# Kernel tuning notes

Hardware: AMD Instinct MI355X
Metric: run time of the kernel (lower is better)

The kernel has to match this reference:

```python
import jax, jax.numpy as jnp
import numpy as np

DN = ('NCHW', 'OIHW', 'NCHW')
COMMITMENT_COST = 0.25


def conv(x, w, b=None, stride=1, pad=0, groups=1):
    o = jax.lax.conv_general_dilated(x, w, (stride, stride), [(pad, pad), (pad, pad)],
                                     feature_group_count=groups, dimension_numbers=DN)
    return o if b is None else o + b[None, :, None, None]


def conv_t(x, w, b=None, stride=2, pad=1, groups=1):
    # w is in torch ConvTranspose2d layout: (in_ch, out_ch//groups, kH, kW)
    in_ch, outg, kh, kw = w.shape
    wf = jnp.flip(w, (-2, -1)).reshape(groups, in_ch // groups, outg, kh, kw)
    wf = wf.transpose(0, 2, 1, 3, 4).reshape(groups * outg, in_ch // groups, kh, kw)
    p = kh - 1 - pad
    o = jax.lax.conv_general_dilated(x, wf, (1, 1), [(p, p), (p, p)],
                                     lhs_dilation=(stride, stride),
                                     feature_group_count=groups, dimension_numbers=DN)
    return o if b is None else o + b[None, :, None, None]


def res_stack(x, w1, w2):
    # w1: (L, nrh, nh//2, 3, 3), w2: (L, nh, nrh//2, 1, 1); groups=2, no bias
    for i in range(w1.shape[0]):
        h = conv(jax.nn.relu(x), w1[i], pad=1, groups=2)
        h = conv(jax.nn.relu(h), w2[i], groups=2)
        x = x + h
    return jax.nn.relu(x)


def vq(z, emb, beta):
    # z: (B, C, H, W); emb: (K, C). EMA updates skipped (eval mode).
    zp = jnp.transpose(z, (0, 2, 3, 1))  # BHWC
    C = emb.shape[1]
    flat = zp.reshape(-1, C)
    d = (jnp.sum(flat ** 2, axis=1, keepdims=True)
         + jnp.sum(emb ** 2, axis=1) - 2.0 * flat @ emb.T)
    idx = jnp.argmin(d, axis=1)
    q = emb[idx].reshape(zp.shape)
    loss = beta * jnp.mean((jax.lax.stop_gradient(q) - zp) ** 2)
    q_st = zp + jax.lax.stop_gradient(q - zp)  # straight-through
    avg = jnp.mean(jax.nn.one_hot(idx, emb.shape[0], dtype=z.dtype), axis=0)
    perplexity = jnp.exp(-jnp.sum(avg * jnp.log(avg + 1e-10)))
    return loss, jnp.transpose(q_st, (0, 3, 1, 2)), perplexity


def _forward(x, eb_dw, eb_db, eb_rw, eb_rb, eb_c1w, eb_c1b, eb_c2w, eb_c2b, eb_c3w, eb_c3b,
             eb_rw1, eb_rw2, et_c1w, et_c1b, et_c2w, et_c2b, et_rw1, et_rw2,
             pvt_w, pvt_b, up_w, up_b, pvb_w, pvb_b, emb_t, emb_b,
             db_c1w, db_c1b, db_rw1, db_rw2, db_t1w, db_t1b, db_t2w, db_t2b,
             db_odw, db_odb, db_orw, db_orb):
    NH = eb_c3w.shape[0]
    ED = emb_t.shape[1]
    # --- EncoderBot ---
    xd = conv(x[:, :1], eb_dw, eb_db)      # depth 1x1 -> NH/4
    xr = conv(x[:, 1:], eb_rw, eb_rb)      # rgb 1x1 -> NH/4
    h = jax.nn.relu(jnp.concatenate([xd, xr], axis=1))
    h = jax.nn.relu(conv(h, eb_c1w, eb_c1b, stride=2, pad=1, groups=2))
    h = jax.nn.relu(conv(h, eb_c2w, eb_c2b, stride=2, pad=1, groups=2))
    h = conv(h, eb_c3w, eb_c3b, pad=1, groups=2)
    enc_b = res_stack(h, eb_rw1, eb_rw2)   # (B, NH, H/4, W/4)
    # --- EncoderTop ---
    t = jax.nn.relu(conv(enc_b, et_c1w, et_c1b, stride=2, pad=1, groups=2))
    t = jax.nn.relu(conv(t, et_c2w, et_c2b, pad=1, groups=2))
    enc_t = res_stack(t, et_rw1, et_rw2)   # (B, NH, H/8, W/8)
    # --- top VQ ---
    zt = conv(enc_t, pvt_w, pvt_b, groups=2)
    loss_t, q_t, perp_t = vq(zt, emb_t, COMMITMENT_COST)
    up_t = conv_t(q_t, up_w, up_b, stride=2, pad=1, groups=2)  # (B, ED, H/4, W/4)
    # --- PreVQBot: regroup channels as (enc_b_d, up_t_d, enc_b_rgb, up_t_rgb) ---
    joined = jnp.concatenate([enc_b[:, :NH // 2], up_t[:, :ED // 2],
                              enc_b[:, NH // 2:], up_t[:, ED // 2:]], axis=1)
    zb = conv(joined, pvb_w, pvb_b, groups=2)
    loss_b, q_b, perp_b = vq(zb, emb_b, COMMITMENT_COST)
    # --- DecoderBot: input cat(up_t, q_b), regrouped (t_d, b_d, t_rgb, b_rgb) ---
    dj = jnp.concatenate([up_t[:, :ED // 2], q_b[:, :ED // 2],
                          up_t[:, ED // 2:], q_b[:, ED // 2:]], axis=1)
    y = conv(dj, db_c1w, db_c1b, pad=1, groups=2)
    y = res_stack(y, db_rw1, db_rw2)
    y = jax.nn.relu(conv_t(y, db_t1w, db_t1b, stride=2, pad=1, groups=2))
    y = conv_t(y, db_t2w, db_t2b, stride=2, pad=1, groups=2)  # (B, NH/4, H, W), no relu
    c = y.shape[1]
    out_d = conv(y[:, :c // 2], db_odw, db_odb)
    out_rgb = conv(y[:, c // 2:], db_orw, db_orb)
    recon = jnp.concatenate([out_d, out_rgb], axis=1)  # (B, 4, H, W)
    return loss_b, loss_t, recon, q_t, q_b


def setup_inputs() -> dict:
    key = jax.random.key(0)
    NH, NRH, L, ED, K = 128, 64, 2, 128, 2048
    B, H, W = 8, 256, 256
    ks = iter(jax.random.split(key, 64))
    def w(*shape):
        return jax.random.normal(next(ks), shape, jnp.float32) * 0.05
    return dict(
        x=jax.random.normal(next(ks), (B, 4, H, W), jnp.float32),
        eb_dw=w(NH // 4, 1, 1, 1), eb_db=w(NH // 4),
        eb_rw=w(NH // 4, 3, 1, 1), eb_rb=w(NH // 4),
        eb_c1w=w(NH // 2, NH // 4, 4, 4), eb_c1b=w(NH // 2),
        eb_c2w=w(NH, NH // 4, 4, 4), eb_c2b=w(NH),
        eb_c3w=w(NH, NH // 2, 3, 3), eb_c3b=w(NH),
        eb_rw1=w(L, NRH, NH // 2, 3, 3), eb_rw2=w(L, NH, NRH // 2, 1, 1),
        et_c1w=w(NH, NH // 2, 4, 4), et_c1b=w(NH),
        et_c2w=w(NH, NH // 2, 3, 3), et_c2b=w(NH),
        et_rw1=w(L, NRH, NH // 2, 3, 3), et_rw2=w(L, NH, NRH // 2, 1, 1),
        pvt_w=w(ED, NH // 2, 1, 1), pvt_b=w(ED),
        up_w=w(ED, ED // 2, 4, 4), up_b=w(ED),
        pvb_w=w(ED, (NH + ED) // 2, 1, 1), pvb_b=w(ED),
        emb_t=jax.random.normal(next(ks), (K, ED), jnp.float32),
        emb_b=jax.random.normal(next(ks), (K, ED), jnp.float32),
        db_c1w=w(NH, ED, 3, 3), db_c1b=w(NH),
        db_rw1=w(L, NRH, NH // 2, 3, 3), db_rw2=w(L, NH, NRH // 2, 1, 1),
        db_t1w=w(NH, NH // 4, 4, 4), db_t1b=w(NH // 2),
        db_t2w=w(NH // 2, NH // 8, 4, 4), db_t2b=w(NH // 4),
        db_odw=w(1, NH // 8, 1, 1), db_odb=w(1),
        db_orw=w(3, NH // 8, 1, 1), db_orb=w(3),
    )


def reference(x, eb_dw, eb_db, eb_rw, eb_rb, eb_c1w, eb_c1b, eb_c2w, eb_c2b, eb_c3w, eb_c3b,
              eb_rw1, eb_rw2, et_c1w, et_c1b, et_c2w, et_c2b, et_rw1, et_rw2,
              pvt_w, pvt_b, up_w, up_b, pvb_w, pvb_b, emb_t, emb_b,
              db_c1w, db_c1b, db_rw1, db_rw2, db_t1w, db_t1b, db_t2w, db_t2b,
              db_odw, db_odb, db_orw, db_orb):
    return _forward(x, eb_dw, eb_db, eb_rw, eb_rb, eb_c1w, eb_c1b, eb_c2w, eb_c2b,
                    eb_c3w, eb_c3b, eb_rw1, eb_rw2, et_c1w, et_c1b, et_c2w, et_c2b,
                    et_rw1, et_rw2, pvt_w, pvt_b, up_w, up_b, pvb_w, pvb_b, emb_t, emb_b,
                    db_c1w, db_c1b, db_rw1, db_rw2, db_t1w, db_t1b, db_t2w, db_t2b,
                    db_odw, db_odb, db_orw, db_orb)
```

## Files before the change

### kernel.cpp

```cpp
#include <hip/hip_runtime.h>
#include <cstddef>

#define TPB 256

__device__ __forceinline__ float4 relu4(float4 v) {
    v.x = fmaxf(v.x, 0.0f); v.y = fmaxf(v.y, 0.0f);
    v.z = fmaxf(v.z, 0.0f); v.w = fmaxf(v.w, 0.0f);
    return v;
}

__device__ __forceinline__ const float* pick_src(const float* a, const float* b,
                                                 int n, int g, int l, int HW) {
    return (l < 64) ? a + ((size_t)n * 128 + g * 64 + l) * HW
                    : b + ((size_t)n * 128 + g * 64 + (l - 64)) * HW;
}

template<int W, int ROWS, int OCB, bool RELU_IN, bool SPLIT>
__global__ __launch_bounds__(256) void conv3_kernel(
    const float* __restrict__ in, const float* __restrict__ in2,
    const float* __restrict__ wgt, const float* __restrict__ bias,
    float* __restrict__ out, int Cin, int Cout, int relu_out)
{
    constexpr int J = ROWS * W / 64;
    constexpr int OCT = OCB * 4;
    constexpr int NW = OCB / 4;
    constexpr int ICB = 8;
    constexpr int IN_H = ROWS + 2, IN_W2 = W + 8;
    constexpr int W4 = W / 4;
    __shared__ float s_in[ICB][IN_H][IN_W2];
    __shared__ float s_w[ICB * 9 * OCT];

    const int tid = threadIdx.x;
    const int tx = tid & 63, ty = tid >> 6;
    const int n = blockIdx.z, oc0 = blockIdx.y * OCT, r0 = blockIdx.x * ROWS;
    const int icg = Cin >> 1, ocg = Cout >> 1;
    const int g = oc0 / ocg;

    float acc[OCB][J];
    #pragma unroll
    for (int o = 0; o < OCB; ++o) {
        const float b = bias ? bias[oc0 + ty * OCB + o] : 0.0f;
        #pragma unroll
        for (int j = 0; j < J; ++j) acc[o][j] = b;
    }

    const float* inb = SPLIT ? nullptr
                             : in + ((size_t)n * Cin + (size_t)g * icg) * (W * W);

    for (int ic0 = 0; ic0 < icg; ic0 += ICB) {
        __syncthreads();
        for (int i = tid; i < ICB * IN_H * W4; i += 256) {
            const int icl = i / (IN_H * W4);
            const int rem = i - icl * (IN_H * W4);
            const int rr = rem / W4, c4 = rem - rr * W4;
            const int y = r0 - 1 + rr;
            float4 v = make_float4(0.f, 0.f, 0.f, 0.f);
            if ((unsigned)y < (unsigned)W) {
                const float* src = SPLIT ? pick_src(in, in2, n, g, ic0 + icl, W * W)
                                         : inb + (size_t)(ic0 + icl) * (W * W);
                v = *(const float4*)(src + (size_t)y * W + 4 * c4);
            }
            if (RELU_IN) v = relu4(v);
            *(float4*)&s_in[icl][rr][4 + 4 * c4] = v;
        }
        for (int i = tid; i < ICB * IN_H; i += 256) {
            const int icl = i / IN_H, rr = i - icl * IN_H;
            s_in[icl][rr][3] = 0.0f;
            s_in[icl][rr][W + 4] = 0.0f;
        }
        for (int i = tid; i < ICB * 9 * OCT; i += 256) {
            const int ocl = i % OCT, rest = i / OCT;
            const int k = rest % 9, icl = rest / 9;
            s_w[i] = wgt[((size_t)(oc0 + ocl) * icg + (ic0 + icl)) * 9 + k];
        }
        __syncthreads();

        #pragma unroll 1
        for (int icl = 0; icl < ICB; ++icl) {
            const float* swb = s_w + icl * 9 * OCT + ty * OCB;
            #pragma unroll
            for (int ky = 0; ky < 3; ++ky) {
                #pragma unroll
                for (int kx = 0; kx < 3; ++kx) {
                    const int kq = ky * 3 + kx;
                    float4 wv[NW];
                    #pragma unroll
                    for (int u = 0; u < NW; ++u)
                        wv[u] = *(const float4*)(swb + kq * OCT + 4 * u);
                    #pragma unroll
                    for (int j = 0; j < J; ++j) {
                        const int p = j * 64 + tx;
                        const int rr = p / W, cc = p - rr * W;
                        const float v = s_in[icl][rr + ky][cc + 3 + kx];
                        #pragma unroll
                        for (int u = 0; u < NW; ++u) {
                            acc[4 * u + 0][j] = fmaf(wv[u].x, v, acc[4 * u + 0][j]);
                            acc[4 * u + 1][j] = fmaf(wv[u].y, v, acc[4 * u + 1][j]);
                            acc[4 * u + 2][j] = fmaf(wv[u].z, v, acc[4 * u + 2][j]);
                            acc[4 * u + 3][j] = fmaf(wv[u].w, v, acc[4 * u + 3][j]);
                        }
                    }
                }
            }
        }
    }

    const int HWo = W * W;
    float* ob = out + ((size_t)n * Cout + oc0 + ty * OCB) * HWo;
    #pragma unroll
    for (int o = 0; o < OCB; ++o) {
        #pragma unroll
        for (int j = 0; j < J; ++j) {
            const int p = j * 64 + tx;
            const int rr = p / W, cc = p - rr * W;
            float r = acc[o][j];
            if (relu_out) r = fmaxf(r, 0.0f);
            ob[(size_t)o * HWo + (size_t)(r0 + rr) * W + cc] = r;
        }
    }
}

template<int W, int ROWS>
__global__ __launch_bounds__(256) void conv4s2_kernel(
    const float* __restrict__ in, const float* __restrict__ wgt,
    const float* __restrict__ bias, float* __restrict__ out,
    int Cin, int Cout, int relu_out)
{
    constexpr int J = ROWS * W / 64;
    constexpr int ICB = 4;
    constexpr int IN_H = 2 * ROWS + 2, IN_W2 = 2 * W + 8;
    constexpr int W24 = W / 2;
    __shared__ float s_in[ICB][IN_H][IN_W2];
    __shared__ float s_w[ICB * 16 * 32];

    const int tid = threadIdx.x;
    const int tx = tid & 63, ty = tid >> 6;
    const int n = blockIdx.z, oc0 = blockIdx.y * 32, r0 = blockIdx.x * ROWS;
    const int icg = Cin >> 1, ocg = Cout >> 1;
    const int g = oc0 / ocg;
    const int Hin = 2 * W;

    float acc[8][J];
    #pragma unroll
    for (int o = 0; o < 8; ++o) {
        const float b = bias ? bias[oc0 + ty * 8 + o] : 0.0f;
        #pragma unroll
        for (int j = 0; j < J; ++j) acc[o][j] = b;
    }

    const float* inb = in + ((size_t)n * Cin + (size_t)g * icg) * (Hin * Hin);
    for (int ic0 = 0; ic0 < icg; ic0 += ICB) {
        __syncthreads();
        for (int i = tid; i < ICB * IN_H * W24; i += 256) {
            const int icl = i / (IN_H * W24);
            const int rem = i - icl * (IN_H * W24);
            const int rr = rem / W24, c4 = rem - rr * W24;
            const int y = 2 * r0 - 1 + rr;
            float4 v = make_float4(0.f, 0.f, 0.f, 0.f);
            if ((unsigned)y < (unsigned)Hin)
                v = *(const float4*)(inb + (size_t)(ic0 + icl) * (Hin * Hin)
                                     + (size_t)y * Hin + 4 * c4);
            *(float4*)&s_in[icl][rr][4 + 4 * c4] = v;
        }
        for (int i = tid; i < ICB * IN_H; i += 256) {
            const int icl = i / IN_H, rr = i - icl * IN_H;
            s_in[icl][rr][3] = 0.0f;
            s_in[icl][rr][2 * W + 4] = 0.0f;
        }
        for (int i = tid; i < ICB * 16 * 32; i += 256) {
            const int ocl = i & 31, rest = i >> 5;
            const int k = rest & 15, icl = rest >> 4;
            s_w[i] = wgt[((size_t)(oc0 + ocl) * icg + (ic0 + icl)) * 16 + k];
        }
        __syncthreads();

        #pragma unroll 1
        for (int icl = 0; icl < ICB; ++icl) {
            const float* swb = s_w + icl * 512 + ty * 8;
            #pragma unroll
            for (int ky = 0; ky < 4; ++ky) {
                #pragma unroll
                for (int kx = 0; kx < 4; ++kx) {
                    const int kq = ky * 4 + kx;
                    const float4 wA = *(const float4*)(swb + kq * 32);
                    const float4 wB = *(const float4*)(swb + kq * 32 + 4);
                    #pragma unroll
                    for (int j = 0; j < J; ++j) {
                        const int p = j * 64 + tx;
                        const int rr = p / W, cc = p - rr * W;
                        const float v = s_in[icl][2 * rr + ky][2 * cc + 3 + kx];
                        acc[0][j] = fmaf(wA.x, v, acc[0][j]);
                        acc[1][j] = fmaf(wA.y, v, acc[1][j]);
                        acc[2][j] = fmaf(wA.z, v, acc[2][j]);
                        acc[3][j] = fmaf(wA.w, v, acc[3][j]);
                        acc[4][j] = fmaf(wB.x, v, acc[4][j]);
                        acc[5][j] = fmaf(wB.y, v, acc[5][j]);
                        acc[6][j] = fmaf(wB.z, v, acc[6][j]);
                        acc[7][j] = fmaf(wB.w, v, acc[7][j]);
                    }
                }
            }
        }
    }

    const int HWo = W * W;
    float* ob = out + ((size_t)n * Cout + oc0 + ty * 8) * HWo;
    #pragma unroll
    for (int o = 0; o < 8; ++o) {
        #pragma unroll
        for (int j = 0; j < J; ++j) {
            const int p = j * 64 + tx;
            const int rr = p / W, cc = p - rr * W;
            float r = acc[o][j];
            if (relu_out) r = fmaxf(r, 0.0f);
            ob[(size_t)o * HWo + (size_t)(r0 + rr) * W + cc] = r;
        }
    }
}

template<int PX, bool RELU_IN, bool ACC, bool RELU_OUT, bool SPLIT>
__global__ __launch_bounds__(256) void conv1_kernel(
    const float* __restrict__ in, const float* __restrict__ in2,
    const float* __restrict__ wgt, const float* __restrict__ bias,
    float* __restrict__ out, int Cin, int Cout, int HW)
{
    constexpr int J = PX / 64;
    constexpr int PX4 = PX / 4;
    constexpr int ICB = 16;
    __shared__ float s_in[ICB][PX];
    __shared__ float s_w[ICB * 32];

    const int tid = threadIdx.x;
    const int tx = tid & 63, ty = tid >> 6;
    const int n = blockIdx.z, oc0 = blockIdx.y * 32, p0 = blockIdx.x * PX;
    const int icg = Cin >> 1, ocg = Cout >> 1;
    const int g = oc0 / ocg;

    float acc[8][J];
    #pragma unroll
    for (int o = 0; o < 8; ++o) {
        const float b = bias ? bias[oc0 + ty * 8 + o] : 0.0f;
        #pragma unroll
        for (int j = 0; j < J; ++j) acc[o][j] = b;
    }

    const float* inb = SPLIT ? nullptr
                             : in + ((size_t)n * Cin + (size_t)g * icg) * HW + p0;
    for (int ic0 = 0; ic0 < icg; ic0 += ICB) {
        __syncthreads();
        for (int i = tid; i < ICB * PX4; i += 256) {
            const int icl = i / PX4, c4 = i - (i / PX4) * PX4;
            const float* src = SPLIT ? pick_src(in, in2, n, g, ic0 + icl, HW) + p0
                                     : inb + (size_t)(ic0 + icl) * HW;
            float4 v = *(const float4*)(src + 4 * c4);
            if (RELU_IN) v = relu4(v);
            *(float4*)&s_in[icl][4 * c4] = v;
        }
        for (int i = tid; i < ICB * 32; i += 256) {
            const int ocl = i & 31, icl = i >> 5;
            s_w[i] = wgt[(size_t)(oc0 + ocl) * icg + ic0 + icl];
        }
        __syncthreads();

        #pragma unroll 4
        for (int icl = 0; icl < ICB; ++icl) {
            const float4 wA = *(const float4*)(s_w + icl * 32 + ty * 8);
            const float4 wB = *(const float4*)(s_w + icl * 32 + ty * 8 + 4);
            #pragma unroll
            for (int j = 0; j < J; ++j) {
                const float v = s_in[icl][j * 64 + tx];
                acc[0][j] = fmaf(wA.x, v, acc[0][j]);
                acc[1][j] = fmaf(wA.y, v, acc[1][j]);
                acc[2][j] = fmaf(wA.z, v, acc[2][j]);
                acc[3][j] = fmaf(wA.w, v, acc[3][j]);
                acc[4][j] = fmaf(wB.x, v, acc[4][j]);
                acc[5][j] = fmaf(wB.y, v, acc[5][j]);
                acc[6][j] = fmaf(wB.z, v, acc[6][j]);
                acc[7][j] = fmaf(wB.w, v, acc[7][j]);
            }
        }
    }

    float* ob = out + ((size_t)n * Cout + oc0 + ty * 8) * HW + p0;
    #pragma unroll
    for (int o = 0; o < 8; ++o) {
        #pragma unroll
        for (int j = 0; j < J; ++j) {
            const size_t idx = (size_t)o * HW + j * 64 + tx;
            float r = acc[o][j];
            if (ACC) r += ob[idx];
            if (RELU_OUT) r = fmaxf(r, 0.0f);
            ob[idx] = r;
        }
    }
}

template<int W, int ROWS, int OCT>
__global__ __launch_bounds__(64 * (OCT / 8)) void convt4_kernel(
    const float* __restrict__ in, const float* __restrict__ wgt,
    const float* __restrict__ bias, float* __restrict__ out,
    int Cin, int Cout, int relu_out)
{
    constexpr int NTHR = 64 * (OCT / 8);
    constexpr int PXT  = ROWS * W / 64;
    constexpr int WP   = W / 64;
    constexpr int ICB  = 8;
    constexpr int RIN  = ((ROWS + 1) >> 1) + 2;
    constexpr int CIN  = W / 2 + 2;
    __shared__ float s_in[ICB][RIN][CIN];
    __shared__ float s_w[ICB * 16 * OCT];

    const int tid = threadIdx.x;
    const int tx = tid & 63, ty = tid >> 6;
    const int n = blockIdx.z;
    const int oc0 = blockIdx.y * OCT;
    const int r0 = blockIdx.x * ROWS;
    const int icg = Cin >> 1, ocg = Cout >> 1;
    const int g = oc0 / ocg, of0 = oc0 - g * ocg;
    const int Hin = W / 2;
    const int iy_lo = (r0 - 2) >> 1;

    float acc[8][PXT];
    #pragma unroll
    for (int o = 0; o < 8; ++o) {
        const float b = bias ? bias[oc0 + ty * 8 + o] : 0.0f;
        #pragma unroll
        for (int j = 0; j < PXT; ++j) acc[o][j] = b;
    }

    const float* inb = in + ((size_t)n * Cin + (size_t)g * icg) * (Hin * Hin);
    const int kxl = ((tx + 1) & 1);
    const int hx  = (tx + 1) >> 1;

    for (int ic0 = 0; ic0 < icg; ic0 += ICB) {
        __syncthreads();
        for (int i = tid; i < ICB * RIN * CIN; i += NTHR) {
            const int icl = i / (RIN * CIN);
            const int rem = i - icl * (RIN * CIN);
            const int rr = rem / CIN, cc = rem - rr * CIN;
            const int y = iy_lo + rr, x = cc - 1;
            float v = 0.0f;
            if ((unsigned)y < (unsigned)Hin && (unsigned)x < (unsigned)Hin)
                v = inb[(size_t)(ic0 + icl) * (Hin * Hin) + y * Hin + x];
            s_in[icl][rr][cc] = v;
        }
        for (int i = tid; i < ICB * 16 * OCT; i += NTHR) {
            const int ocl = i & (OCT - 1);
            const int rest = i / OCT;
            const int k = rest & 15, icl = rest >> 4;
            s_w[i] = wgt[((size_t)(g * icg + ic0 + icl) * ocg + of0 + ocl) * 16 + k];
        }
        __syncthreads();

        #pragma unroll 1
        for (int icl = 0; icl < ICB; ++icl) {
            const float* swb = s_w + icl * 16 * OCT + ty * 8;
            #pragma unroll
            for (int tt = 0; tt < 4; ++tt) {
                const int ty2 = tt >> 1, tx2 = tt & 1;
                float4 wp0[2], wp1[2];
                #pragma unroll
                for (int par = 0; par < 2; ++par) {
                    const int koff = ((2 * ty2 + par) * 4 + (kxl + 2 * tx2)) * OCT;
                    wp0[par] = *(const float4*)(swb + koff);
                    wp1[par] = *(const float4*)(swb + koff + 4);
                }
                const int cbase = hx - tx2 + 1;
                #pragma unroll
                for (int j = 0; j < PXT; ++j) {
                    const int row_j = j / WP, m_j = j - row_j * WP;
                    const int pj = (row_j + 1) & 1;
                    const int rloc = (row_j + 1 - pj) / 2 - ty2 + 1;
                    const float v = s_in[icl][rloc][32 * m_j + cbase];
                    const float4 wa = pj ? wp0[1] : wp0[0];
                    const float4 wb = pj ? wp1[1] : wp1[0];
                    acc[0][j] = fmaf(wa.x, v, acc[0][j]);
                    acc[1][j] = fmaf(wa.y, v, acc[1][j]);
                    acc[2][j] = fmaf(wa.z, v, acc[2][j]);
                    acc[3][j] = fmaf(wa.w, v, acc[3][j]);
                    acc[4][j] = fmaf(wb.x, v, acc[4][j]);
                    acc[5][j] = fmaf(wb.y, v, acc[5][j]);
                    acc[6][j] = fmaf(wb.z, v, acc[6][j]);
                    acc[7][j] = fmaf(wb.w, v, acc[7][j]);
                }
            }
        }
    }

    const int HWo = W * W;
    float* ob = out + ((size_t)n * Cout + oc0 + ty * 8) * HWo;
    #pragma unroll
    for (int o = 0; o < 8; ++o) {
        #pragma unroll
        for (int j = 0; j < PXT; ++j) {
            const int row_j = j / WP, m_j = j - row_j * WP;
            float r = acc[o][j];
            if (relu_out) r = fmaxf(r, 0.0f);
            ob[(size_t)o * HWo + (size_t)(r0 + row_j) * W + 64 * m_j + tx] = r;
        }
    }
}

__global__ void head_kernel(const float* __restrict__ x,
                            const float* __restrict__ dw, const float* __restrict__ db,
                            const float* __restrict__ rw, const float* __restrict__ rb,
                            float* __restrict__ out)
{
    const int idx = blockIdx.x * TPB + threadIdx.x;
    const int HW4 = 16384;
    if (idx >= 8 * 64 * HW4) return;
    const int p4 = idx & (HW4 - 1);
    const int t = idx >> 14;
    const int c = t & 63, n = t >> 6;
    const float4* xb4 = (const float4*)(x + (size_t)n * 4 * 65536);
    float4 v;
    if (c < 32) {
        const float w = dw[c], b = db[c];
        const float4 d = xb4[p4];
        v.x = fmaf(d.x, w, b); v.y = fmaf(d.y, w, b);
        v.z = fmaf(d.z, w, b); v.w = fmaf(d.w, w, b);
    } else {
        const int cc = c - 32;
        const float w0 = rw[cc * 3], w1 = rw[cc * 3 + 1], w2 = rw[cc * 3 + 2];
        const float b = rb[cc];
        const float4 r = xb4[HW4 + p4], g4 = xb4[2 * HW4 + p4], bl = xb4[3 * HW4 + p4];
        v.x = fmaf(bl.x, w2, fmaf(g4.x, w1, fmaf(r.x, w0, b)));
        v.y = fmaf(bl.y, w2, fmaf(g4.y, w1, fmaf(r.y, w0, b)));
        v.z = fmaf(bl.z, w2, fmaf(g4.z, w1, fmaf(r.z, w0, b)));
        v.w = fmaf(bl.w, w2, fmaf(g4.w, w1, fmaf(r.w, w0, b)));
    }
    ((float4*)out)[idx] = relu4(v);
}

__global__ void emb_norm_kernel(const float* __restrict__ emb, float* __restrict__ en, int K)
{
    const int k = blockIdx.x * TPB + threadIdx.x;
    if (k >= K) return;
    const float4* e = (const float4*)(emb + (size_t)k * 128);
    float s = 0.0f;
    for (int c = 0; c < 32; ++c) {
        const float4 t = e[c];
        s = fmaf(t.x, t.x, s); s = fmaf(t.y, t.y, s);
        s = fmaf(t.z, t.z, s); s = fmaf(t.w, t.w, s);
    }
    en[k] = s;
}

#define VQ_TV 64
#define VQ_TE 64
__global__ __launch_bounds__(256) void vq_kernel(
    const float* __restrict__ z, const float* __restrict__ emb,
    const float* __restrict__ en_g,
    float* __restrict__ q, float* __restrict__ lossp,
    int HW, int Kc)
{
    __shared__ float zs[32][65][4];
    __shared__ float es[32][65][4];
    __shared__ float en[VQ_TE];
    __shared__ float rdd[VQ_TV][16];
    __shared__ int   rdi[VQ_TV][16];
    __shared__ int   idxv[VQ_TV];
    __shared__ float red[256];

    const int tid = threadIdx.x;
    const int vg = tid >> 4, eg = tid & 15;
    const long long gv0 = (long long)blockIdx.x * VQ_TV;
    const int n = (int)(gv0 / HW);
    const int p0 = (int)(gv0 - (long long)n * HW);
    const float* zb = z + (size_t)n * 128 * HW + p0;

    for (int i = tid; i < 64 * 128; i += 256) {
        const int v = i & 63, c = i >> 6;
        zs[c >> 2][v][c & 3] = zb[(size_t)c * HW + v];
    }
    __syncthreads();

    float best[4]; int bidx[4];
    #pragma unroll
    for (int r = 0; r < 4; ++r) { best[r] = 1e30f; bidx[r] = 0; }

    for (int e0 = 0; e0 < Kc; e0 += VQ_TE) {
        for (int i = tid; i < VQ_TE * 128; i += 256) {
            const int c = i & 127, el = i >> 7;
            es[c >> 2][el][c & 3] = emb[(size_t)(e0 + el) * 128 + c];
        }
        if (tid < VQ_TE) en[tid] = en_g[e0 + tid];
        __syncthreads();

        float dot[4][4];
        #pragma unroll
        for (int r = 0; r < 4; ++r)
            #pragma unroll
            for (int s = 0; s < 4; ++s) dot[r][s] = 0.0f;

        for (int c4 = 0; c4 < 32; ++c4) {
            float4 zr[4], ee[4];
            #pragma unroll
            for (int r = 0; r < 4; ++r) zr[r] = *(const float4*)&zs[c4][4 * vg + r][0];
            #pragma unroll
            for (int s = 0; s < 4; ++s) ee[s] = *(const float4*)&es[c4][eg + 16 * s][0];
            #pragma unroll
            for (int r = 0; r < 4; ++r) {
                #pragma unroll
                for (int s = 0; s < 4; ++s) {
                    dot[r][s] = fmaf(zr[r].x, ee[s].x, dot[r][s]);
                    dot[r][s] = fmaf(zr[r].y, ee[s].y, dot[r][s]);
                    dot[r][s] = fmaf(zr[r].z, ee[s].z, dot[r][s]);
                    dot[r][s] = fmaf(zr[r].w, ee[s].w, dot[r][s]);
                }
            }
        }
        #pragma unroll
        for (int s = 0; s < 4; ++s) {
            const float e2 = en[eg + 16 * s];
            const int ei = e0 + eg + 16 * s;
            #pragma unroll
            for (int r = 0; r < 4; ++r) {
                const float d = e2 - 2.0f * dot[r][s];
                if (d < best[r]) { best[r] = d; bidx[r] = ei; }
            }
        }
        __syncthreads();
    }

    #pragma unroll
    for (int r = 0; r < 4; ++r) { rdd[4 * vg + r][eg] = best[r]; rdi[4 * vg + r][eg] = bidx[r]; }
    __syncthreads();
    if (tid < VQ_TV) {
        float bd = rdd[tid][0]; int bi = rdi[tid][0];
        for (int j = 1; j < 16; ++j) {
            const float d = rdd[tid][j]; const int i2 = rdi[tid][j];
            if (d < bd || (d == bd && i2 < bi)) { bd = d; bi = i2; }
        }
        idxv[tid] = bi;
    }
    __syncthreads();

    float ls = 0.0f;
    float* qb = q + (size_t)n * 128 * HW + p0;
    for (int i = tid; i < 64 * 128; i += 256) {
        const int v = i & 63, c = i >> 6;
        const float e = emb[(size_t)idxv[v] * 128 + c];
        qb[(size_t)c * HW + v] = e;
        const float diff = e - zs[c >> 2][v][c & 3];
        ls = fmaf(diff, diff, ls);
    }
    red[tid] = ls;
    __syncthreads();
    for (int s = 128; s > 0; s >>= 1) {
        if (tid < s) red[tid] += red[tid + s];
        __syncthreads();
    }
    if (tid == 0) lossp[blockIdx.x] = red[0];
}

__global__ void loss_finish_kernel(const float* __restrict__ p, int n, float scale,
                                   float* __restrict__ out)
{
    __shared__ float red[256];
    float s = 0.0f;
    for (int i = threadIdx.x; i < n; i += 256) s += p[i];
    red[threadIdx.x] = s;
    __syncthreads();
    for (int k = 128; k > 0; k >>= 1) {
        if (threadIdx.x < k) red[threadIdx.x] += red[threadIdx.x + k];
        __syncthreads();
    }
    if (threadIdx.x == 0) out[0] = red[0] * scale;
}

__global__ void outconv_kernel(const float* __restrict__ y,
                               const float* __restrict__ odw, const float* __restrict__ odb,
                               const float* __restrict__ orw, const float* __restrict__ orb,
                               float* __restrict__ out)
{
    const int idx = blockIdx.x * TPB + threadIdx.x;
    const int HW4 = 16384;
    if (idx >= 8 * 4 * HW4) return;
    const int p4 = idx & (HW4 - 1);
    const int t = idx >> 14;
    const int c = t & 3, n = t >> 2;
    const float4* yb4 = (const float4*)(y + (size_t)n * 32 * 65536);
    float4 v;
    const int base = (c == 0) ? 0 : 16;
    const float* wv = (c == 0) ? odw : orw + (c - 1) * 16;
    const float b = (c == 0) ? odb[0] : orb[c - 1];
    v.x = b; v.y = b; v.z = b; v.w = b;
    for (int k = 0; k < 16; ++k) {
        const float w = wv[k];
        const float4 f = yb4[(size_t)(base + k) * HW4 + p4];
        v.x = fmaf(f.x, w, v.x); v.y = fmaf(f.y, w, v.y);
        v.z = fmaf(f.z, w, v.z); v.w = fmaf(f.w, w, v.w);
    }
    ((float4*)out)[idx] = v;
}

extern "C" void kernel_launch(void* const* d_in, const int* in_sizes, int n_in,
                              void* d_out, int out_size, void* d_ws, size_t ws_size,
                              hipStream_t stream)
{
    const float* x      = (const float*)d_in[0];
    const float* eb_dw  = (const float*)d_in[1];
    const float* eb_db  = (const float*)d_in[2];
    const float* eb_rw  = (const float*)d_in[3];
    const float* eb_rb  = (const float*)d_in[4];
    const float* eb_c1w = (const float*)d_in[5];
    const float* eb_c1b = (const float*)d_in[6];
    const float* eb_c2w = (const float*)d_in[7];
    const float* eb_c2b = (const float*)d_in[8];
    const float* eb_c3w = (const float*)d_in[9];
    const float* eb_c3b = (const float*)d_in[10];
    const float* eb_rw1 = (const float*)d_in[11];
    const float* eb_rw2 = (const float*)d_in[12];
    const float* et_c1w = (const float*)d_in[13];
    const float* et_c1b = (const float*)d_in[14];
    const float* et_c2w = (const float*)d_in[15];
    const float* et_c2b = (const float*)d_in[16];
    const float* et_rw1 = (const float*)d_in[17];
    const float* et_rw2 = (const float*)d_in[18];
    const float* pvt_w  = (const float*)d_in[19];
    const float* pvt_b  = (const float*)d_in[20];
    const float* up_w   = (const float*)d_in[21];
    const float* up_b   = (const float*)d_in[22];
    const float* pvb_w  = (const float*)d_in[23];
    const float* pvb_b  = (const float*)d_in[24];
    const float* emb_t  = (const float*)d_in[25];
    const float* emb_b  = (const float*)d_in[26];
    const float* db_c1w = (const float*)d_in[27];
    const float* db_c1b = (const float*)d_in[28];
    const float* db_rw1 = (const float*)d_in[29];
    const float* db_rw2 = (const float*)d_in[30];
    const float* db_t1w = (const float*)d_in[31];
    const float* db_t1b = (const float*)d_in[32];
    const float* db_t2w = (const float*)d_in[33];
    const float* db_t2b = (const float*)d_in[34];
    const float* db_odw = (const float*)d_in[35];
    const float* db_odb = (const float*)d_in[36];
    const float* db_orw = (const float*)d_in[37];
    const float* db_orb = (const float*)d_in[38];

    float* ws  = (float*)d_ws;
    float* out = (float*)d_out;

    const size_t OFF_H0   = 0;
    const size_t OFF_H1   = 33554432;
    const size_t OFF_H2   = 0;
    const size_t OFF_ENCB = 4194304;
    const size_t OFF_RH   = 8388608;
    const size_t OFF_T1   = 10485760;
    const size_t OFF_T2   = 11534336;
    const size_t OFF_ZT   = 12582912;
    const size_t OFF_UPT  = 13631488;
    const size_t OFF_ZB   = 17825792;
    const size_t OFF_Y    = 22020096;
    const size_t OFF_Y1   = 26214400;
    const size_t OFF_Y2   = 0;
    const size_t OFF_ENT  = 34603008;
    const size_t OFF_ENB  = 34605056;
    const size_t OFF_LPT  = 34607104;
    const size_t OFF_LPB  = 34607232;
    const size_t NEED     = 41943680;
    if (ws_size < NEED * sizeof(float)) return;

    float* o_loss_b = out + 0;
    float* o_loss_t = out + 1;
    float* o_recon  = out + 2;
    float* o_qt     = out + 2 + 8 * 4 * 65536;
    float* o_qb     = o_qt + 8 * 128 * 1024;

    head_kernel<<<8 * 64 * 16384 / TPB, TPB, 0, stream>>>(
        x, eb_dw, eb_db, eb_rw, eb_rb, ws + OFF_H0);
    conv4s2_kernel<128, 2><<<dim3(64, 2, 8), 256, 0, stream>>>(
        ws + OFF_H0, eb_c1w, eb_c1b, ws + OFF_H1, 64, 64, 1);
    conv4s2_kernel<64, 4><<<dim3(16, 4, 8), 256, 0, stream>>>(
        ws + OFF_H1, eb_c2w, eb_c2b, ws + OFF_H2, 64, 128, 1);
    emb_norm_kernel<<<8, TPB, 0, stream>>>(emb_t, ws + OFF_ENT, 2048);
    emb_norm_kernel<<<8, TPB, 0, stream>>>(emb_b, ws + OFF_ENB, 2048);
    conv3_kernel<64, 4, 8, false, false><<<dim3(16, 4, 8), 256, 0, stream>>>(
        ws + OFF_H2, nullptr, eb_c3w, eb_c3b, ws + OFF_ENCB, 128, 128, 0);
    for (int i = 0; i < 2; ++i) {
        conv3_kernel<64, 4, 4, true, false><<<dim3(16, 4, 8), 256, 0, stream>>>(
            ws + OFF_ENCB, nullptr, eb_rw1 + (size_t)i * 64 * 64 * 9, nullptr,
            ws + OFF_RH, 128, 64, 0);
        if (i == 1)
            conv1_kernel<256, true, true, true, false><<<dim3(16, 4, 8), 256, 0, stream>>>(
                ws + OFF_RH, nullptr, eb_rw2 + (size_t)i * 128 * 32, nullptr,
                ws + OFF_ENCB, 64, 128, 4096);
        else
            conv1_kernel<256, true, true, false, false><<<dim3(16, 4, 8), 256, 0, stream>>>(
                ws + OFF_RH, nullptr, eb_rw2 + (size_t)i * 128 * 32, nullptr,
                ws + OFF_ENCB, 64, 128, 4096);
    }

    conv4s2_kernel<32, 4><<<dim3(8, 4, 8), 256, 0, stream>>>(
        ws + OFF_ENCB, et_c1w, et_c1b, ws + OFF_T1, 128, 128, 1);
    conv3_kernel<32, 4, 8, false, false><<<dim3(8, 4, 8), 256, 0, stream>>>(
        ws + OFF_T1, nullptr, et_c2w, et_c2b, ws + OFF_T2, 128, 128, 1);
    for (int i = 0; i < 2; ++i) {
        conv3_kernel<32, 4, 4, true, false><<<dim3(8, 4, 8), 256, 0, stream>>>(
            ws + OFF_T2, nullptr, et_rw1 + (size_t)i * 64 * 64 * 9, nullptr,
            ws + OFF_RH, 128, 64, 0);
        if (i == 1)
            conv1_kernel<128, true, true, true, false><<<dim3(8, 4, 8), 256, 0, stream>>>(
                ws + OFF_RH, nullptr, et_rw2 + (size_t)i * 128 * 32, nullptr,
                ws + OFF_T2, 64, 128, 1024);
        else
            conv1_kernel<128, true, true, false, false><<<dim3(8, 4, 8), 256, 0, stream>>>(
                ws + OFF_RH, nullptr, et_rw2 + (size_t)i * 128 * 32, nullptr,
                ws + OFF_T2, 64, 128, 1024);
    }

    conv1_kernel<128, false, false, false, false><<<dim3(8, 4, 8), 256, 0, stream>>>(
        ws + OFF_T2, nullptr, pvt_w, pvt_b, ws + OFF_ZT, 128, 128, 1024);
    vq_kernel<<<128, 256, 0, stream>>>(ws + OFF_ZT, emb_t, ws + OFF_ENT, o_qt,
                                       ws + OFF_LPT, 1024, 2048);
    loss_finish_kernel<<<1, 256, 0, stream>>>(ws + OFF_LPT, 128,
                                              0.25f / (8192.0f * 128.0f), o_loss_t);

    convt4_kernel<64, 4, 32><<<dim3(16, 4, 8), 256, 0, stream>>>(
        o_qt, up_w, up_b, ws + OFF_UPT, 128, 128, 0);

    conv1_kernel<256, false, false, false, true><<<dim3(16, 4, 8), 256, 0, stream>>>(
        ws + OFF_ENCB, ws + OFF_UPT, pvb_w, pvb_b, ws + OFF_ZB, 256, 128, 4096);
    vq_kernel<<<512, 256, 0, stream>>>(ws + OFF_ZB, emb_b, ws + OFF_ENB, o_qb,
                                       ws + OFF_LPB, 4096, 2048);
    loss_finish_kernel<<<1, 256, 0, stream>>>(ws + OFF_LPB, 512,
                                              0.25f / (32768.0f * 128.0f), o_loss_b);

    conv3_kernel<64, 4, 8, false, true><<<dim3(16, 4, 8), 256, 0, stream>>>(
        ws + OFF_UPT, o_qb, db_c1w, db_c1b, ws + OFF_Y, 256, 128, 0);
    for (int i = 0; i < 2; ++i) {
        conv3_kernel<64, 4, 4, true, false><<<dim3(16, 4, 8), 256, 0, stream>>>(
            ws + OFF_Y, nullptr, db_rw1 + (size_t)i * 64 * 64 * 9, nullptr,
            ws + OFF_RH, 128, 64, 0);
        if (i == 1)
            conv1_kernel<256, true, true, true, false><<<dim3(16, 4, 8), 256, 0, stream>>>(
                ws + OFF_RH, nullptr, db_rw2 + (size_t)i * 128 * 32, nullptr,
                ws + OFF_Y, 64, 128, 4096);
        else
            conv1_kernel<256, true, true, false, false><<<dim3(16, 4, 8), 256, 0, stream>>>(
                ws + OFF_RH, nullptr, db_rw2 + (size_t)i * 128 * 32, nullptr,
                ws + OFF_Y, 64, 128, 4096);
    }
    convt4_kernel<128, 2, 32><<<dim3(64, 2, 8), 256, 0, stream>>>(
        ws + OFF_Y, db_t1w, db_t1b, ws + OFF_Y1, 128, 64, 1);
    convt4_kernel<256, 2, 16><<<dim3(128, 2, 8), 128, 0, stream>>>(
        ws + OFF_Y1, db_t2w, db_t2b, ws + OFF_Y2, 64, 32, 0);
    outconv_kernel<<<8 * 4 * 16384 / TPB, TPB, 0, stream>>>(
        ws + OFF_Y2, db_odw, db_odb, db_orw, db_orb, o_recon);
}
```

Baseline: 1.762 ms.

## Add register-tiled VQ kernel for bottom codebook and widen conv3 output-channel blocking

Adds a vq2 kernel for the bottom codebook. Each block handles 128 vectors and stages 128-code embedding tiles in shared memory, with each thread computing an 8x8 register tile of dot products before a shuffle-based argmin reduction. It also writes the quantized output and computes the loss with float4 stores. Separately, the 64-wide conv3 launches double OCB and halve the channel-group grid dimension, so each block reuses input tiles across more output channels. The trade-off is higher register and shared-memory pressure and fewer blocks.

```diff
diff --git a/kernel.cpp b/kernel.cpp
--- a/kernel.cpp
+++ b/kernel.cpp
@@ -544,6 +544,127 @@
         qb[(size_t)c * HW + v] = e;
         const float diff = e - zs[c >> 2][v][c & 3];
         ls = fmaf(diff, diff, ls);
+    }
+    red[tid] = ls;
+    __syncthreads();
+    for (int s = 128; s > 0; s >>= 1) {
+        if (tid < s) red[tid] += red[tid + s];
+        __syncthreads();
+    }
+    if (tid == 0) lossp[blockIdx.x] = red[0];
+}
+
+__global__ __launch_bounds__(256) void vq2_kernel(
+    const float* __restrict__ z, const float* __restrict__ emb,
+    const float* __restrict__ en_g,
+    float* __restrict__ q, float* __restrict__ lossp,
+    int HW, int Kc)
+{
+    __shared__ float zs[32][129][4];
+    __shared__ float es[32][129][4];
+    __shared__ float en[128];
+    __shared__ int   idxv[128];
+    __shared__ float red[256];
+
+    const int tid = threadIdx.x;
+    const int vg = tid >> 4, eg = tid & 15;
+    const long long gv0 = (long long)blockIdx.x * 128;
+    const int n = (int)(gv0 / HW);
+    const int p0 = (int)(gv0 - (long long)n * HW);
+    const float* zb = z + (size_t)n * 128 * HW + p0;
+
+    for (int i = tid; i < 128 * 32; i += 256) {
+        const int c = i >> 5, v4 = i & 31;
+        const float4 t = *(const float4*)(zb + (size_t)c * HW + 4 * v4);
+        zs[c >> 2][4 * v4 + 0][c & 3] = t.x;
+        zs[c >> 2][4 * v4 + 1][c & 3] = t.y;
+        zs[c >> 2][4 * v4 + 2][c & 3] = t.z;
+        zs[c >> 2][4 * v4 + 3][c & 3] = t.w;
+    }
+    __syncthreads();
+
+    float best[8]; int bidx[8];
+    #pragma unroll
+    for (int r = 0; r < 8; ++r) { best[r] = 1e30f; bidx[r] = 0; }
+
+    for (int e0 = 0; e0 < Kc; e0 += 128) {
+        __syncthreads();
+        for (int i = tid; i < 128 * 32; i += 256) {
+            const int e = i >> 5, c4i = i & 31;
+            const float4 t = *(const float4*)(emb + (size_t)(e0 + e) * 128 + 4 * c4i);
+            *(float4*)&es[c4i][e][0] = t;
+        }
+        if (tid < 128) en[tid] = en_g[e0 + tid];
+        __syncthreads();
+
+        float dot[8][8];
+        #pragma unroll
+        for (int r = 0; r < 8; ++r)
+            #pragma unroll
+            for (int s = 0; s < 8; ++s) dot[r][s] = 0.0f;
+
+        for (int c4 = 0; c4 < 32; ++c4) {
+            float4 zr[8], ee[8];
+            #pragma unroll
+            for (int r = 0; r < 8; ++r) zr[r] = *(const float4*)&zs[c4][vg + 16 * r][0];
+            #pragma unroll
+            for (int s = 0; s < 8; ++s) ee[s] = *(const float4*)&es[c4][eg + 16 * s][0];
+            #pragma unroll
+            for (int r = 0; r < 8; ++r) {
+                #pragma unroll
+                for (int s = 0; s < 8; ++s) {
+                    dot[r][s] = fmaf(zr[r].x, ee[s].x, dot[r][s]);
+                    dot[r][s] = fmaf(zr[r].y, ee[s].y, dot[r][s]);
+                    dot[r][s] = fmaf(zr[r].z, ee[s].z, dot[r][s]);
+                    dot[r][s] = fmaf(zr[r].w, ee[s].w, dot[r][s]);
+                }
+            }
+        }
+        #pragma unroll
+        for (int s = 0; s < 8; ++s) {
+            const float e2 = en[eg + 16 * s];
+            const int ei = e0 + eg + 16 * s;
+            #pragma unroll
+            for (int r = 0; r < 8; ++r) {
+                const float d = e2 - 2.0f * dot[r][s];
+                if (d < best[r]) { best[r] = d; bidx[r] = ei; }
+            }
+        }
+    }
+
+    #pragma unroll
+    for (int off = 8; off > 0; off >>= 1) {
+        #pragma unroll
+        for (int r = 0; r < 8; ++r) {
+            const float d2 = __shfl_down(best[r], (unsigned)off, 16);
+            const int   i2 = __shfl_down(bidx[r], (unsigned)off, 16);
+            if (d2 < best[r] || (d2 == best[r] && i2 < bidx[r])) {
+                best[r] = d2; bidx[r] = i2;
+            }
+        }
+    }
+    if (eg == 0) {
+        #pragma unroll
+        for (int r = 0; r < 8; ++r) idxv[vg + 16 * r] = bidx[r];
+    }
+    __syncthreads();
+
+    float ls = 0.0f;
+    float* qb = q + (size_t)n * 128 * HW + p0;
+    for (int i = tid; i < 128 * 32; i += 256) {
+        const int c = i >> 5, v4 = i & 31;
+        float4 e4;
+        e4.x = emb[(size_t)idxv[4 * v4 + 0] * 128 + c];
+        e4.y = emb[(size_t)idxv[4 * v4 + 1] * 128 + c];
+        e4.z = emb[(size_t)idxv[4 * v4 + 2] * 128 + c];
+        e4.w = emb[(size_t)idxv[4 * v4 + 3] * 128 + c];
+        *(float4*)(qb + (size_t)c * HW + 4 * v4) = e4;
+        const float d0 = e4.x - zs[c >> 2][4 * v4 + 0][c & 3];
+        const float d1 = e4.y - zs[c >> 2][4 * v4 + 1][c & 3];
+        const float d2 = e4.z - zs[c >> 2][4 * v4 + 2][c & 3];
+        const float d3 = e4.w - zs[c >> 2][4 * v4 + 3][c & 3];
+        ls = fmaf(d0, d0, ls); ls = fmaf(d1, d1, ls);
+        ls = fmaf(d2, d2, ls); ls = fmaf(d3, d3, ls);
     }
     red[tid] = ls;
     __syncthreads();
@@ -676,10 +797,10 @@
         ws + OFF_H1, eb_c2w, eb_c2b, ws + OFF_H2, 64, 128, 1);
     emb_norm_kernel<<<8, TPB, 0, stream>>>(emb_t, ws + OFF_ENT, 2048);
     emb_norm_kernel<<<8, TPB, 0, stream>>>(emb_b, ws + OFF_ENB, 2048);
-    conv3_kernel<64, 4, 8, false, false><<<dim3(16, 4, 8), 256, 0, stream>>>(
+    conv3_kernel<64, 4, 16, false, false><<<dim3(16, 2, 8), 256, 0, stream>>>(
         ws + OFF_H2, nullptr, eb_c3w, eb_c3b, ws + OFF_ENCB, 128, 128, 0);
     for (int i = 0; i < 2; ++i) {
-        conv3_kernel<64, 4, 4, true, false><<<dim3(16, 4, 8), 256, 0, stream>>>(
+        conv3_kernel<64, 4, 8, true, false><<<dim3(16, 2, 8), 256, 0, stream>>>(
             ws + OFF_ENCB, nullptr, eb_rw1 + (size_t)i * 64 * 64 * 9, nullptr,
             ws + OFF_RH, 128, 64, 0);
         if (i == 1)
@@ -722,15 +843,15 @@
 
     conv1_kernel<256, false, false, false, true><<<dim3(16, 4, 8), 256, 0, stream>>>(
         ws + OFF_ENCB, ws + OFF_UPT, pvb_w, pvb_b, ws + OFF_ZB, 256, 128, 4096);
-    vq_kernel<<<512, 256, 0, stream>>>(ws + OFF_ZB, emb_b, ws + OFF_ENB, o_qb,
-                                       ws + OFF_LPB, 4096, 2048);
-    loss_finish_kernel<<<1, 256, 0, stream>>>(ws + OFF_LPB, 512,
+    vq2_kernel<<<256, 256, 0, stream>>>(ws + OFF_ZB, emb_b, ws + OFF_ENB, o_qb,
+                                        ws + OFF_LPB, 4096, 2048);
+    loss_finish_kernel<<<1, 256, 0, stream>>>(ws + OFF_LPB, 256,
                                               0.25f / (32768.0f * 128.0f), o_loss_b);
 
-    conv3_kernel<64, 4, 8, false, true><<<dim3(16, 4, 8), 256, 0, stream>>>(
+    conv3_kernel<64, 4, 16, false, true><<<dim3(16, 2, 8), 256, 0, stream>>>(
         ws + OFF_UPT, o_qb, db_c1w, db_c1b, ws + OFF_Y, 256, 128, 0);
     for (int i = 0; i < 2; ++i) {
-        conv3_kernel<64, 4, 4, true, false><<<dim3(16, 4, 8), 256, 0, stream>>>(
+        conv3_kernel<64, 4, 8, true, false><<<dim3(16, 2, 8), 256, 0, stream>>>(
             ws + OFF_Y, nullptr, db_rw1 + (size_t)i * 64 * 64 * 9, nullptr,
             ws + OFF_RH, 128, 64, 0);
         if (i == 1)
```

After: 1.879 ms, median of 3. +6.6%, slower.
